# Performance work log

Hardware: AMD Instinct MI355X
Metric: run time of the kernel (lower is better)

## Reference

```python
import jax, jax.numpy as jnp
import numpy as np

N = 50000          # nodes
E = 800000         # edges (avg degree 16)
F_IN = 64          # raw node features
H = 128            # hidden width (n_hidden[0..5])
H6 = 256           # n_hidden[6]
H7 = 128           # n_hidden[7]
EDGE_DIM = 21


def _lin(k, fan_in, fan_out):
    return jax.random.normal(k, (fan_in, fan_out), jnp.float32) * (1.0 / np.sqrt(fan_in))


def setup_inputs() -> dict:
    key = jax.random.key(0)
    ks = jax.random.split(key, 32)
    inp = {
        "G": jax.random.normal(ks[0], (N, F_IN), jnp.float32),
        "edge_index": jax.random.randint(ks[1], (2, E), 0, N, jnp.int32),
        "edge_attr": jax.random.normal(ks[2], (E, EDGE_DIM), jnp.float32),
        # MLP embedding
        "We1": _lin(ks[3], F_IN, H), "be1": jnp.zeros((H,), jnp.float32),
        "We2": _lin(ks[4], H, H),    "be2": jnp.zeros((H,), jnp.float32),
        "We3": _lin(ks[5], H, H),    "be3": jnp.zeros((H,), jnp.float32),
        # conv1 (ResGatedGraphConv, edge_dim=21)
        "c1_Wk": _lin(ks[6], H, H),  "c1_bk": jnp.zeros((H,), jnp.float32),
        "c1_Wq": _lin(ks[7], H, H),  "c1_bq": jnp.zeros((H,), jnp.float32),
        "c1_Wv": _lin(ks[8], H, H),  "c1_bv": jnp.zeros((H,), jnp.float32),
        "c1_We": _lin(ks[9], EDGE_DIM, H),
        "c1_Ws": _lin(ks[10], H, H), "c1_bs": jnp.zeros((H,), jnp.float32),
        # conv2
        "c2_Wk": _lin(ks[11], H, H), "c2_bk": jnp.zeros((H,), jnp.float32),
        "c2_Wq": _lin(ks[12], H, H), "c2_bq": jnp.zeros((H,), jnp.float32),
        "c2_Wv": _lin(ks[13], H, H), "c2_bv": jnp.zeros((H,), jnp.float32),
        "c2_We": _lin(ks[14], EDGE_DIM, H),
        "c2_Ws": _lin(ks[15], H, H), "c2_bs": jnp.zeros((H,), jnp.float32),
        # graph-level MLP
        "Wg1": _lin(ks[16], H, H),   "bg1": jnp.zeros((H,), jnp.float32),
        "Wg2": _lin(ks[17], H, H),   "bg2": jnp.zeros((H,), jnp.float32),
        # head (input is concat(node_emb, graph_mean) -> 2*H)
        "Wl1": _lin(ks[18], 2 * H, H6), "bl1": jnp.zeros((H6,), jnp.float32),
        "Wl2": _lin(ks[19], H6, H7),    "bl2": jnp.zeros((H7,), jnp.float32),
        "Wl3": _lin(ks[20], H7, 1),     "bl3": jnp.zeros((1,), jnp.float32),
    }
    return inp


def _res_gated_conv(x, src, dst, ea, Wk, bk, Wq, bq, Wv, bv, We, Ws, bs):
    """PyG ResGatedGraphConv with edge_dim:
    msg = sigmoid((k_i + e) + (q_j + e)) * (v_j + e), scatter-add to target i."""
    k = x @ Wk + bk            # [N,H] keys (target side)
    q = x @ Wq + bq            # [N,H] queries (source side)
    v = x @ Wv + bv            # [N,H] values (source side)
    e = ea @ We                # [E,H] edge transform (no bias)
    gate = jax.nn.sigmoid(k[dst] + q[src] + 2.0 * e)   # [E,H]
    msg = gate * (v[src] + e)                           # [E,H]
    agg = jax.ops.segment_sum(msg, dst, num_segments=x.shape[0])
    return agg + x @ Ws + bs   # root/skip connection


def reference(G, edge_index, edge_attr,
              We1, be1, We2, be2, We3, be3,
              c1_Wk, c1_bk, c1_Wq, c1_bq, c1_Wv, c1_bv, c1_We, c1_Ws, c1_bs,
              c2_Wk, c2_bk, c2_Wq, c2_bq, c2_Wv, c2_bv, c2_We, c2_Ws, c2_bs,
              Wg1, bg1, Wg2, bg2,
              Wl1, bl1, Wl2, bl2, Wl3, bl3):
    src, dst = edge_index[0], edge_index[1]
    h = jax.nn.relu(G @ We1 + be1)
    h = jax.nn.relu(h @ We2 + be2)
    h = jax.nn.relu(h @ We3 + be3)
    h = jax.nn.relu(_res_gated_conv(h, src, dst, edge_attr,
                                    c1_Wk, c1_bk, c1_Wq, c1_bq, c1_Wv, c1_bv,
                                    c1_We, c1_Ws, c1_bs))
    h = jax.nn.relu(_res_gated_conv(h, src, dst, edge_attr,
                                    c2_Wk, c2_bk, c2_Wq, c2_bq, c2_Wv, c2_bv,
                                    c2_We, c2_Ws, c2_bs))
    h = jax.nn.relu(h @ Wg1 + bg1)
    h = h @ Wg2 + bg2                      # [N,H]
    gmean = jnp.mean(h, axis=0)            # graph embedding [H]
    u = jnp.concatenate([h, jnp.broadcast_to(gmean, h.shape)], axis=-1)  # [N,2H]
    u = jax.nn.relu(u @ Wl1 + bl1)
    u = jax.nn.relu(u @ Wl2 + bl2)
    u = (u @ Wl3 + bl3).squeeze(-1)        # [N] per-node scalar logits
    return u
```

## Files before the change

### kernel.cpp

```cpp
#include <hip/hip_runtime.h>
#include <hip/hip_fp16.h>

#define NN 50000
#define NE 800000
#define HH 128
#define SCAN_BS 512
#define SCAN_NB 98
#define LDK 40
#define LDA 136
#define LDU 264

typedef _Float16 half8 __attribute__((ext_vector_type(8)));
typedef float f32x4  __attribute__((ext_vector_type(4)));

__global__ __launch_bounds__(256)
void presplit_w(const float* __restrict__ s0,  const float* __restrict__ s1,
                const float* __restrict__ s2,  const float* __restrict__ s3,
                const float* __restrict__ s4,  const float* __restrict__ s5,
                const float* __restrict__ s6,  const float* __restrict__ s7,
                const float* __restrict__ s8,  const float* __restrict__ s9,
                const float* __restrict__ s10, const float* __restrict__ s11,
                const float* __restrict__ s12, const float* __restrict__ s13,
                const float* __restrict__ s14, _Float16* __restrict__ wps)
{
    const float* srcs[15] = {s0,s1,s2,s3,s4,s5,s6,s7,s8,s9,s10,s11,s12,s13,s14};
    const int Ks[15]   = {64,128,128,128,128,128,128,128,128,128,128,128,128,128,256};
    const int logKs[15]= { 6,  7,  7,  7,  7,  7,  7,  7,  7,  7,  7,  7,  7,  7,  8};
    const int off[15]  = {0,8192,24576,40960,57344,73728,90112,106496,122880,
                          139264,155648,172032,188416,204800,237568};

    const int mi = blockIdx.y;
    const float* src = srcs[mi];
    const int K = Ks[mi], logK = logKs[mi];
    const int N = (mi == 13) ? 256 : 128;
    _Float16* dst = wps + off[mi];
    const int tot = K * N;
    const int base = (blockIdx.x * 256 + threadIdx.x) * 4;
    if (base >= tot) return;
    const int n = base >> logK;
    const int k = base & (K - 1);
#pragma unroll
    for (int x = 0; x < 4; ++x)
        dst[(size_t)n * K + k + x] = (_Float16)src[(size_t)(k + x) * N + n];
}

template<bool RELU>
__device__ __forceinline__ void layer_l2l(
    const _Float16* __restrict__ actA, int lda, int K,
    const _Float16* __restrict__ Bt,
    const float* __restrict__ bias,
    _Float16* __restrict__ actO, int ldo, int oc0,
    _Float16* __restrict__ Bs)
{
    const int t = threadIdx.x, lane = t & 63;
    const int wr = (t >> 6) >> 1, wc = (t >> 6) & 1;
    const int fr = lane & 15, fg = lane >> 4;
    const int rb = t >> 1, kb = (t & 1) * 16;

    f32x4 acc[2][4] = {};
    for (int k0 = 0; k0 < K; k0 += 32) {
        const _Float16* p = Bt + (size_t)rb * K + k0 + kb;
        const half8 v0 = *reinterpret_cast<const half8*>(p);
        const half8 v1 = *reinterpret_cast<const half8*>(p + 8);
        *reinterpret_cast<half8*>(&Bs[rb * LDK + kb])     = v0;
        *reinterpret_cast<half8*>(&Bs[rb * LDK + kb + 8]) = v1;
        __syncthreads();

        half8 a[2], b[4];
#pragma unroll
        for (int i = 0; i < 2; ++i)
            a[i] = *reinterpret_cast<const half8*>(&actA[(wr * 32 + i * 16 + fr) * lda + k0 + fg * 8]);
#pragma unroll
        for (int j = 0; j < 4; ++j)
            b[j] = *reinterpret_cast<const half8*>(&Bs[(wc * 64 + j * 16 + fr) * LDK + fg * 8]);
#pragma unroll
        for (int i = 0; i < 2; ++i)
#pragma unroll
            for (int j = 0; j < 4; ++j)
                acc[i][j] = __builtin_amdgcn_mfma_f32_16x16x32_f16(a[i], b[j], acc[i][j], 0, 0, 0);
        __syncthreads();
    }
#pragma unroll
    for (int j = 0; j < 4; ++j) {
        const int gnl = wc * 64 + j * 16 + fr;
        const float bv = bias[gnl];
#pragma unroll
        for (int i = 0; i < 2; ++i)
#pragma unroll
            for (int rr = 0; rr < 4; ++rr) {
                float v = acc[i][j][rr] + bv;
                if (RELU) v = fmaxf(v, 0.f);
                actO[(wr * 32 + i * 16 + fg * 4 + rr) * ldo + oc0 + gnl] = (_Float16)v;
            }
    }
    __syncthreads();
}

__global__ __launch_bounds__(256)
void mlp3_kernel(const float* __restrict__ G,
                 const _Float16* __restrict__ W1, const float* __restrict__ b1,
                 const _Float16* __restrict__ W2, const float* __restrict__ b2,
                 const _Float16* __restrict__ W3, const float* __restrict__ b3,
                 _Float16* __restrict__ outf, int M)
{
    __shared__ __attribute__((aligned(16))) _Float16 AA[64 * LDA];
    __shared__ __attribute__((aligned(16))) _Float16 AB[64 * LDA];
    __shared__ __attribute__((aligned(16))) _Float16 Bs[128 * LDK];

    const int t  = threadIdx.x;
    const int m0 = blockIdx.x << 6;

    {
        const int r  = t >> 2;
        const int c0 = (t & 3) * 16;
        const int gm = m0 + r;
#pragma unroll
        for (int h = 0; h < 2; ++h) {
            float4 v0 = make_float4(0.f, 0.f, 0.f, 0.f), v1 = v0;
            if (gm < M) {
                v0 = *reinterpret_cast<const float4*>(G + (size_t)gm * 64 + c0 + h * 8);
                v1 = *reinterpret_cast<const float4*>(G + (size_t)gm * 64 + c0 + h * 8 + 4);
            }
            half8 hv;
            hv[0] = (_Float16)v0.x; hv[1] = (_Float16)v0.y;
            hv[2] = (_Float16)v0.z; hv[3] = (_Float16)v0.w;
            hv[4] = (_Float16)v1.x; hv[5] = (_Float16)v1.y;
            hv[6] = (_Float16)v1.z; hv[7] = (_Float16)v1.w;
            *reinterpret_cast<half8*>(&AA[r * LDA + c0 + h * 8]) = hv;
        }
    }
    __syncthreads();

    layer_l2l<true>(AA, LDA, 64,  W1, b1, AB, LDA, 0, Bs);
    layer_l2l<true>(AB, LDA, 128, W2, b2, AA, LDA, 0, Bs);
    layer_l2l<true>(AA, LDA, 128, W3, b3, AB, LDA, 0, Bs);

    {
        const int r  = t >> 2;
        const int c0 = (t & 3) * 32;
        const int gm = m0 + r;
        if (gm < M) {
#pragma unroll
            for (int x = 0; x < 32; x += 8)
                *reinterpret_cast<half8*>(outf + (size_t)gm * 128 + c0 + x) =
                    *reinterpret_cast<const half8*>(&AB[r * LDA + c0 + x]);
        }
    }
}

__global__ __launch_bounds__(256)
void kqvs_kernel(const _Float16* __restrict__ act,
                 const _Float16* __restrict__ B0, const _Float16* __restrict__ B1,
                 const _Float16* __restrict__ B2, const _Float16* __restrict__ B3,
                 const float* __restrict__ b0, const float* __restrict__ b1,
                 const float* __restrict__ b2, const float* __restrict__ b3,
                 _Float16* __restrict__ ksb, _Float16* __restrict__ qvb, int M)
{
    __shared__ __attribute__((aligned(16))) _Float16 AA[64 * LDA];
    __shared__ __attribute__((aligned(16))) _Float16 Bs[128 * LDK];

    const int t  = threadIdx.x, lane = t & 63;
    const int m0 = blockIdx.x << 6;
    const int wr = (t >> 6) >> 1, wc = (t >> 6) & 1;
    const int fr = lane & 15, fg = lane >> 4;
    const int rb = t >> 1, kb = (t & 1) * 16;

    {
        const int r  = t >> 2;
        const int c0 = (t & 3) * 32;
        const int gm = m0 + r;
#pragma unroll
        for (int x = 0; x < 32; x += 8) {
            half8 v = {0,0,0,0,0,0,0,0};
            if (gm < M) v = *reinterpret_cast<const half8*>(act + (size_t)gm * 128 + c0 + x);
            *reinterpret_cast<half8*>(&AA[r * LDA + c0 + x]) = v;
        }
    }
    __syncthreads();

#pragma unroll
    for (int nb = 0; nb < 4; ++nb) {
        const _Float16* Bt = (nb == 0) ? B0 : (nb == 1) ? B1 : (nb == 2) ? B2 : B3;
        const float*    bt = (nb == 0) ? b0 : (nb == 1) ? b1 : (nb == 2) ? b2 : b3;
        _Float16* dst = (nb < 2) ? ksb : qvb;
        const int sub = (nb & 1) * 2;

        f32x4 acc[2][4] = {};
        for (int k0 = 0; k0 < 128; k0 += 32) {
            const _Float16* p = Bt + (size_t)rb * 128 + k0 + kb;
            const half8 v0 = *reinterpret_cast<const half8*>(p);
            const half8 v1 = *reinterpret_cast<const half8*>(p + 8);
            *reinterpret_cast<half8*>(&Bs[rb * LDK + kb])     = v0;
            *reinterpret_cast<half8*>(&Bs[rb * LDK + kb + 8]) = v1;
            __syncthreads();

            half8 a[2], b[4];
#pragma unroll
            for (int i = 0; i < 2; ++i)
                a[i] = *reinterpret_cast<const half8*>(&AA[(wr * 32 + i * 16 + fr) * LDA + k0 + fg * 8]);
#pragma unroll
            for (int j = 0; j < 4; ++j)
                b[j] = *reinterpret_cast<const half8*>(&Bs[(wc * 64 + j * 16 + fr) * LDK + fg * 8]);
#pragma unroll
            for (int i = 0; i < 2; ++i)
#pragma unroll
                for (int j = 0; j < 4; ++j)
                    acc[i][j] = __builtin_amdgcn_mfma_f32_16x16x32_f16(a[i], b[j], acc[i][j], 0, 0, 0);
            __syncthreads();
        }
#pragma unroll
        for (int j = 0; j < 4; ++j) {
            const int gnl = wc * 64 + j * 16 + fr;
            const int pos = ((gnl >> 1) << 2) + sub + (gnl & 1);
            const float bv = bt[gnl];
#pragma unroll
            for (int i = 0; i < 2; ++i) {
                const int mbase = m0 + wr * 32 + i * 16 + fg * 4;
#pragma unroll
                for (int rr = 0; rr < 4; ++rr) {
                    const int gm = mbase + rr;
                    if (gm < M)
                        dst[(size_t)gm * 256 + pos] = (_Float16)(acc[i][j][rr] + bv);
                }
            }
        }
    }
}

__global__ __launch_bounds__(256)
void graph2_kernel(const _Float16* __restrict__ act,
                   const _Float16* __restrict__ Wg1t, const float* __restrict__ bg1,
                   const _Float16* __restrict__ Wg2t, const float* __restrict__ bg2,
                   _Float16* __restrict__ g2f, float* __restrict__ gsum, int M)
{
    __shared__ __attribute__((aligned(16))) _Float16 AA[64 * LDA];
    __shared__ __attribute__((aligned(16))) _Float16 AB[64 * LDA];
    __shared__ __attribute__((aligned(16))) _Float16 Bs[128 * LDK];

    const int t  = threadIdx.x, lane = t & 63;
    const int m0 = blockIdx.x << 6;
    const int wr = (t >> 6) >> 1, wc = (t >> 6) & 1;
    const int fr = lane & 15, fg = lane >> 4;
    const int rb = t >> 1, kb = (t & 1) * 16;

    {
        const int r  = t >> 2;
        const int c0 = (t & 3) * 32;
        const int gm = m0 + r;
#pragma unroll
        for (int x = 0; x < 32; x += 8) {
            half8 v = {0,0,0,0,0,0,0,0};
            if (gm < M) v = *reinterpret_cast<const half8*>(act + (size_t)gm * 128 + c0 + x);
            *reinterpret_cast<half8*>(&AA[r * LDA + c0 + x]) = v;
        }
    }
    __syncthreads();

    layer_l2l<true>(AA, LDA, 128, Wg1t, bg1, AB, LDA, 0, Bs);

    f32x4 acc[2][4] = {};
    for (int k0 = 0; k0 < 128; k0 += 32) {
        const _Float16* p = Wg2t + (size_t)rb * 128 + k0 + kb;
        const half8 v0 = *reinterpret_cast<const half8*>(p);
        const half8 v1 = *reinterpret_cast<const half8*>(p + 8);
        *reinterpret_cast<half8*>(&Bs[rb * LDK + kb])     = v0;
        *reinterpret_cast<half8*>(&Bs[rb * LDK + kb + 8]) = v1;
        __syncthreads();
        half8 a[2], b[4];
#pragma unroll
        for (int i = 0; i < 2; ++i)
            a[i] = *reinterpret_cast<const half8*>(&AB[(wr * 32 + i * 16 + fr) * LDA + k0 + fg * 8]);
#pragma unroll
        for (int j = 0; j < 4; ++j)
            b[j] = *reinterpret_cast<const half8*>(&Bs[(wc * 64 + j * 16 + fr) * LDK + fg * 8]);
#pragma unroll
        for (int i = 0; i < 2; ++i)
#pragma unroll
            for (int j = 0; j < 4; ++j)
                acc[i][j] = __builtin_amdgcn_mfma_f32_16x16x32_f16(a[i], b[j], acc[i][j], 0, 0, 0);
        __syncthreads();
    }
#pragma unroll
    for (int j = 0; j < 4; ++j) {
        const int gn = wc * 64 + j * 16 + fr;
        const float bv = bg2[gn];
        float csum = 0.f;
#pragma unroll
        for (int i = 0; i < 2; ++i) {
            const int mbase = m0 + wr * 32 + i * 16 + fg * 4;
#pragma unroll
            for (int rr = 0; rr < 4; ++rr) {
                const int gm = mbase + rr;
                if (gm < M) {
                    const float v = acc[i][j][rr] + bv;
                    csum += v;
                    g2f[(size_t)gm * 128 + gn] = (_Float16)v;
                }
            }
        }
        csum += __shfl_xor(csum, 16);
        csum += __shfl_xor(csum, 32);
        if (fg == 0) atomicAdd(&gsum[gn], csum);
    }
}

__global__ __launch_bounds__(256)
void head3_kernel(const _Float16* __restrict__ g2f,
                  const _Float16* __restrict__ Wl1t,
                  const float* __restrict__ gvec,
                  const _Float16* __restrict__ Wl2t,
                  const float* __restrict__ bl2,
                  const float* __restrict__ wl3,
                  const float* __restrict__ bl3,
                  float* __restrict__ out, int M)
{
    __shared__ __attribute__((aligned(16))) _Float16 AA[64 * LDA];
    __shared__ __attribute__((aligned(16))) _Float16 UB[64 * LDU];
    __shared__ __attribute__((aligned(16))) _Float16 Bs[128 * LDK];
    __shared__ float psum[2][64];

    const int t  = threadIdx.x, lane = t & 63;
    const int m0 = blockIdx.x << 6;
    const int wr = (t >> 6) >> 1, wc = (t >> 6) & 1;
    const int fr = lane & 15, fg = lane >> 4;
    const int rb = t >> 1, kb = (t & 1) * 16;

    {
        const int r  = t >> 2;
        const int c0 = (t & 3) * 32;
        const int gm = m0 + r;
#pragma unroll
        for (int x = 0; x < 32; x += 8) {
            half8 v = {0,0,0,0,0,0,0,0};
            if (gm < M) v = *reinterpret_cast<const half8*>(g2f + (size_t)gm * 128 + c0 + x);
            *reinterpret_cast<half8*>(&AA[r * LDA + c0 + x]) = v;
        }
    }
    __syncthreads();

    layer_l2l<true>(AA, LDA, 128, Wl1t,             gvec,       UB, LDU, 0,   Bs);
    layer_l2l<true>(AA, LDA, 128, Wl1t + 128 * 128, gvec + 128, UB, LDU, 128, Bs);

    f32x4 acc[2][4] = {};
    for (int k0 = 0; k0 < 256; k0 += 32) {
        const _Float16* p = Wl2t + (size_t)rb * 256 + k0 + kb;
        const half8 v0 = *reinterpret_cast<const half8*>(p);
        const half8 v1 = *reinterpret_cast<const half8*>(p + 8);
        *reinterpret_cast<half8*>(&Bs[rb * LDK + kb])     = v0;
        *reinterpret_cast<half8*>(&Bs[rb * LDK + kb + 8]) = v1;
        __syncthreads();
        half8 a[2], b[4];
#pragma unroll
        for (int i = 0; i < 2; ++i)
            a[i] = *reinterpret_cast<const half8*>(&UB[(wr * 32 + i * 16 + fr) * LDU + k0 + fg * 8]);
#pragma unroll
        for (int j = 0; j < 4; ++j)
            b[j] = *reinterpret_cast<const half8*>(&Bs[(wc * 64 + j * 16 + fr) * LDK + fg * 8]);
#pragma unroll
        for (int i = 0; i < 2; ++i)
#pragma unroll
            for (int j = 0; j < 4; ++j)
                acc[i][j] = __builtin_amdgcn_mfma_f32_16x16x32_f16(a[i], b[j], acc[i][j], 0, 0, 0);
        __syncthreads();
    }

    float p[2][4] = {};
#pragma unroll
    for (int j = 0; j < 4; ++j) {
        const int gnl = wc * 64 + j * 16 + fr;
        const float bv = bl2[gnl];
        const float wv = wl3[gnl];
#pragma unroll
        for (int i = 0; i < 2; ++i)
#pragma unroll
            for (int rr = 0; rr < 4; ++rr)
                p[i][rr] += fmaxf(acc[i][j][rr] + bv, 0.f) * wv;
    }
#pragma unroll
    for (int i = 0; i < 2; ++i)
#pragma unroll
        for (int rr = 0; rr < 4; ++rr) {
            float s = p[i][rr];
            s += __shfl_xor(s, 1);
            s += __shfl_xor(s, 2);
            s += __shfl_xor(s, 4);
            s += __shfl_xor(s, 8);
            p[i][rr] = s;
        }
    if (fr == 0) {
#pragma unroll
        for (int i = 0; i < 2; ++i)
#pragma unroll
            for (int rr = 0; rr < 4; ++rr)
                psum[wc][wr * 32 + i * 16 + fg * 4 + rr] = p[i][rr];
    }
    __syncthreads();
    if (t < 64) {
        const int gm = m0 + t;
        if (gm < M) out[gm] = psum[0][t] + psum[1][t] + bl3[0];
    }
}

__global__ __launch_bounds__(256)
void hist_kernel(const int* __restrict__ ei, int* __restrict__ deg)
{
    const int e = blockIdx.x * 256 + threadIdx.x;
    if (e < NE) atomicAdd(&deg[ei[NE + e]], 1);
}

__global__ __launch_bounds__(SCAN_BS)
void scan1_kernel(const int* __restrict__ deg, int* __restrict__ incl,
                  int* __restrict__ bsum)
{
    __shared__ int sm[SCAN_BS];
    const int t = threadIdx.x;
    const int i = blockIdx.x * SCAN_BS + t;
    sm[t] = (i < NN) ? deg[i] : 0;
    __syncthreads();
    for (int d = 1; d < SCAN_BS; d <<= 1) {
        const int add = (t >= d) ? sm[t - d] : 0;
        __syncthreads();
        sm[t] += add;
        __syncthreads();
    }
    if (i < NN) incl[i] = sm[t];
    if (t == SCAN_BS - 1) bsum[blockIdx.x] = sm[t];
}

__global__ __launch_bounds__(128)
void scan2_kernel(int* __restrict__ bsum)
{
    __shared__ int sm[128];
    const int t = threadIdx.x;
    const int v = (t < SCAN_NB) ? bsum[t] : 0;
    sm[t] = v;
    __syncthreads();
    for (int d = 1; d < 128; d <<= 1) {
        const int add = (t >= d) ? sm[t - d] : 0;
        __syncthreads();
        sm[t] += add;
        __syncthreads();
    }
    if (t < SCAN_NB) bsum[t] = sm[t] - v;
}

__global__ __launch_bounds__(SCAN_BS)
void scan3_kernel(const int* __restrict__ incl, const int* __restrict__ deg,
                  const int* __restrict__ bsum, int* __restrict__ offs)
{
    const int t = threadIdx.x;
    const int i = blockIdx.x * SCAN_BS + t;
    if (i < NN) offs[i] = incl[i] - deg[i] + bsum[blockIdx.x];
    if (i == 0) offs[NN] = NE;
}

__global__ __launch_bounds__(256)
void scatter_kernel(const int* __restrict__ ei, const int* __restrict__ offs,
                    int* __restrict__ cur,
                    int* __restrict__ csr_src, int* __restrict__ csr_eid)
{
    const int e = blockIdx.x * 256 + threadIdx.x;
    if (e >= NE) return;
    const int d = ei[NE + e];
    const int p = offs[d] + atomicAdd(&cur[d], 1);
    csr_src[p] = ei[e];
    csr_eid[p] = e;
}

__global__ __launch_bounds__(256)
void build_ea2(const int* __restrict__ csr_eid, const float* __restrict__ ea,
               unsigned* __restrict__ ea2)
{
    const int j = blockIdx.x * 256 + threadIdx.x;
    if (j >= NE) return;
    const int eid = csr_eid[j];
    const float* src = ea + (size_t)eid * 21;
    unsigned* dst = ea2 + (size_t)j * 21;
#pragma unroll
    for (int q = 0; q < 21; ++q) {
        const __half2 h = __floats2half2_rn(src[q], src[q]);
        dst[q] = __builtin_bit_cast(unsigned, h);
    }
}

__global__ __launch_bounds__(256, 8)
void conv_agg_kernel(const int* __restrict__ offs,
                     const int* __restrict__ csr_src,
                     const unsigned* __restrict__ ea2,
                     const float* __restrict__ We,
                     const _Float16* __restrict__ ksb,
                     const _Float16* __restrict__ qvb,
                     _Float16* __restrict__ outh)
{
    const int t    = threadIdx.x;
    const int lane = t & 63;
    const int n    = blockIdx.x * 4 + (t >> 6);
    if (n >= NN) return;

    __half2 w2[21];
#pragma unroll
    for (int q = 0; q < 21; ++q) {
        const float2 wq = *reinterpret_cast<const float2*>(&We[q * HH + 2 * lane]);
        w2[q] = __floats2half2_rn(wq.x, wq.y);
    }

    const uint2 ks = *reinterpret_cast<const uint2*>(ksb + (size_t)n * 256 + lane * 4);
    const __half2 k2 = __builtin_bit_cast(__half2, ks.x);
    const __half2 s2 = __builtin_bit_cast(__half2, ks.y);
    const __half2 one2 = __float2half2_rn(1.f);
    const __half2 two2 = __float2half2_rn(2.f);

    const int j0 = __builtin_amdgcn_readfirstlane(offs[n]);
    const int j1 = __builtin_amdgcn_readfirstlane(offs[n + 1]);
    float acc0 = 0.f, acc1 = 0.f;

#define GATHER(S) (*reinterpret_cast<const uint2*>(qvb + (size_t)(S) * 256 + lane * 4))

#define EDGE(QV, J) { \
    const __half2* aa_ = reinterpret_cast<const __half2*>(ea2 + (size_t)(J) * 21); \
    __half2 e01_ = __float2half2_rn(0.f); \
    _Pragma("unroll") \
    for (int q_ = 0; q_ < 21; ++q_) e01_ = __hfma2(aa_[q_], w2[q_], e01_); \
    const __half2 q2_ = __builtin_bit_cast(__half2, (QV).x); \
    const __half2 v2_ = __builtin_bit_cast(__half2, (QV).y); \
    const __half2 g_  = __hadd2(k2, __hfma2(two2, e01_, q2_)); \
    const __half2 ex_ = h2exp(__hneg2(g_)); \
    const __half2 gate_ = h2rcp(__hadd2(one2, ex_)); \
    const __half2 m_ = __hmul2(gate_, __hadd2(v2_, e01_)); \
    acc0 += __low2float(m_); \
    acc1 += __high2float(m_); }

    int j = j0;
    for (; j + 4 <= j1; j += 4) {
        const int sa = csr_src[j],     sb = csr_src[j + 1];
        const int sc = csr_src[j + 2], sd = csr_src[j + 3];
        const uint2 qva = GATHER(sa);
        const uint2 qvb_ = GATHER(sb);
        const uint2 qvc = GATHER(sc);
        const uint2 qvd = GATHER(sd);
        EDGE(qva, j)
        EDGE(qvb_, j + 1)
        EDGE(qvc, j + 2)
        EDGE(qvd, j + 3)
    }
    for (; j < j1; ++j) {
        const int s_ = csr_src[j];
        const uint2 qv = GATHER(s_);
        EDGE(qv, j)
    }
#undef GATHER
#undef EDGE

    const float r0 = fmaxf(acc0 + __low2float(s2), 0.f);
    const float r1 = fmaxf(acc1 + __high2float(s2), 0.f);
    const __half2 res = __floats2half2_rn(r0, r1);
    *reinterpret_cast<__half2*>(outh + (size_t)n * HH + 2 * lane) = res;
}

__global__ __launch_bounds__(256)
void gvec_kernel(const float* __restrict__ gsum,
                 const float* __restrict__ Wl1,
                 const float* __restrict__ bl1,
                 float* __restrict__ gvec, float invM)
{
    const int j = threadIdx.x;
    float acc = bl1[j];
    for (int k = 0; k < 128; ++k)
        acc += (gsum[k] * invM) * Wl1[(size_t)(128 + k) * 256 + j];
    gvec[j] = acc;
}

extern "C" void kernel_launch(void* const* d_in, const int* in_sizes, int n_in,
                              void* d_out, int out_size, void* d_ws, size_t ws_size,
                              hipStream_t stream)
{
    const float* G   = (const float*)d_in[0];
    const int*   ei  = (const int*)  d_in[1];
    const float* ea  = (const float*)d_in[2];
    const float* We1 = (const float*)d_in[3];  const float* be1 = (const float*)d_in[4];
    const float* We2 = (const float*)d_in[5];  const float* be2 = (const float*)d_in[6];
    const float* We3 = (const float*)d_in[7];  const float* be3 = (const float*)d_in[8];
    const float* c1_Wk = (const float*)d_in[9];  const float* c1_bk = (const float*)d_in[10];
    const float* c1_Wq = (const float*)d_in[11]; const float* c1_bq = (const float*)d_in[12];
    const float* c1_Wv = (const float*)d_in[13]; const float* c1_bv = (const float*)d_in[14];
    const float* c1_We = (const float*)d_in[15];
    const float* c1_Ws = (const float*)d_in[16]; const float* c1_bs = (const float*)d_in[17];
    const float* c2_Wk = (const float*)d_in[18]; const float* c2_bk = (const float*)d_in[19];
    const float* c2_Wq = (const float*)d_in[20]; const float* c2_bq = (const float*)d_in[21];
    const float* c2_Wv = (const float*)d_in[22]; const float* c2_bv = (const float*)d_in[23];
    const float* c2_We = (const float*)d_in[24];
    const float* c2_Ws = (const float*)d_in[25]; const float* c2_bs = (const float*)d_in[26];
    const float* Wg1 = (const float*)d_in[27]; const float* bg1 = (const float*)d_in[28];
    const float* Wg2 = (const float*)d_in[29]; const float* bg2 = (const float*)d_in[30];
    const float* Wl1 = (const float*)d_in[31]; const float* bl1 = (const float*)d_in[32];
    const float* Wl2 = (const float*)d_in[33]; const float* bl2 = (const float*)d_in[34];
    const float* Wl3 = (const float*)d_in[35]; const float* bl3 = (const float*)d_in[36];

    float* out = (float*)d_out;

    char* ws = (char*)d_ws;
    size_t off = 0;
    _Float16* wps  = (_Float16*)(ws + off); off += 270336 * 2;
    _Float16* hA   = (_Float16*)(ws + off); off += (size_t)NN * 128 * 2;
    _Float16* hB   = (_Float16*)(ws + off); off += (size_t)NN * 128 * 2;
    _Float16* ksb  = (_Float16*)(ws + off); off += (size_t)NN * 256 * 2;
    _Float16* qvb  = (_Float16*)(ws + off); off += (size_t)NN * 256 * 2;
    unsigned* ea2  = (unsigned*)(ws + off); off += (size_t)NE * 21 * 4;
    int*      deg  = (int*)     (ws + off); off += (size_t)NN * 4;
    int*      cur  = (int*)     (ws + off); off += (size_t)NN * 4;
    float*    gsum = (float*)   (ws + off); off += 256 * 4;
    float*    gvec = (float*)   (ws + off); off += 256 * 4;
    int*      incl = (int*)     (ws + off); off += (size_t)NN * 4;
    int*      bsum = (int*)     (ws + off); off += 128 * 4;
    int*      offs = (int*)     (ws + off); off += (size_t)(NN + 2) * 4;
    int*      csr_src = (int*)  (ws + off); off += (size_t)NE * 4;
    int*      csr_eid = (int*)  (ws + off); off += (size_t)NE * 4;

    const int O_We1 = 0,      O_We2 = 8192,   O_We3 = 24576;
    const int O_c1k = 40960,  O_c1s = 57344,  O_c1q = 73728,  O_c1v = 90112;
    const int O_c2k = 106496, O_c2s = 122880, O_c2q = 139264, O_c2v = 155648;
    const int O_Wg1 = 172032, O_Wg2 = 188416, O_Wl1 = 204800, O_Wl2 = 237568;

    const dim3 blk(256);
    const int  MT = (NN + 63) / 64;
    const int  EB = (NE + 255) / 256;
    const int  AGGB = (NN + 3) / 4;

    presplit_w<<<dim3(32, 15), blk, 0, stream>>>(
        We1, We2, We3, c1_Wk, c1_Ws, c1_Wq, c1_Wv,
        c2_Wk, c2_Ws, c2_Wq, c2_Wv, Wg1, Wg2, Wl1, Wl2, wps);

    hipMemsetAsync(deg, 0, (size_t)(2 * NN + 256) * 4, stream);
    hist_kernel<<<dim3(EB), blk, 0, stream>>>(ei, deg);
    scan1_kernel<<<dim3(SCAN_NB), dim3(SCAN_BS), 0, stream>>>(deg, incl, bsum);
    scan2_kernel<<<dim3(1), dim3(128), 0, stream>>>(bsum);
    scan3_kernel<<<dim3(SCAN_NB), dim3(SCAN_BS), 0, stream>>>(incl, deg, bsum, offs);
    scatter_kernel<<<dim3(EB), blk, 0, stream>>>(ei, offs, cur, csr_src, csr_eid);
    build_ea2<<<dim3(EB), blk, 0, stream>>>(csr_eid, ea, ea2);

    mlp3_kernel<<<dim3(MT), blk, 0, stream>>>(G,
        wps + O_We1, be1, wps + O_We2, be2, wps + O_We3, be3, hA, NN);

    kqvs_kernel<<<dim3(MT), blk, 0, stream>>>(hA,
        wps + O_c1k, wps + O_c1s, wps + O_c1q, wps + O_c1v,
        c1_bk, c1_bs, c1_bq, c1_bv, ksb, qvb, NN);
    conv_agg_kernel<<<dim3(AGGB), blk, 0, stream>>>(offs, csr_src, ea2, c1_We,
        ksb, qvb, hB);

    kqvs_kernel<<<dim3(MT), blk, 0, stream>>>(hB,
        wps + O_c2k, wps + O_c2s, wps + O_c2q, wps + O_c2v,
        c2_bk, c2_bs, c2_bq, c2_bv, ksb, qvb, NN);
    conv_agg_kernel<<<dim3(AGGB), blk, 0, stream>>>(offs, csr_src, ea2, c2_We,
        ksb, qvb, hA);

    graph2_kernel<<<dim3(MT), blk, 0, stream>>>(hA,
        wps + O_Wg1, bg1, wps + O_Wg2, bg2, hB, gsum, NN);

    gvec_kernel<<<dim3(1), dim3(256), 0, stream>>>(gsum, Wl1, bl1, gvec, 1.f / NN);

    head3_kernel<<<dim3(MT), blk, 0, stream>>>(hB,
        wps + O_Wl1, gvec, wps + O_Wl2, bl2, Wl3, bl3, out, NN);
}
```

Measured before the change: 516.1 us.

## Merge graph-prep kernels with weight split and MLP, fold sigmoid into exp2

Merges the degree histogram into the weight-presplit launch, and merges the CSR scatter and edge-attribute conversion into the MLP embedding launch as extra blocks. Each edge now writes its converted attributes straight to its CSR slot, which removes the csr_eid array, one kernel and two launches. The k and q projections are pre-scaled by -log2(e), so the gate uses exp2 with no negation. This drops an instruction per edge, but the ea2 writes become scattered and the scaled values run through fp16 with a little more rounding.

```diff
diff --git a/kernel.cpp b/kernel.cpp
--- a/kernel.cpp
+++ b/kernel.cpp
@@ -9,33 +9,42 @@
 #define LDK 40
 #define LDA 136
 #define LDU 264
+#define EBLK ((NE + 255) / 256)
 
 typedef _Float16 half8 __attribute__((ext_vector_type(8)));
 typedef float f32x4  __attribute__((ext_vector_type(4)));
 
 __global__ __launch_bounds__(256)
-void presplit_w(const float* __restrict__ s0,  const float* __restrict__ s1,
-                const float* __restrict__ s2,  const float* __restrict__ s3,
-                const float* __restrict__ s4,  const float* __restrict__ s5,
-                const float* __restrict__ s6,  const float* __restrict__ s7,
-                const float* __restrict__ s8,  const float* __restrict__ s9,
-                const float* __restrict__ s10, const float* __restrict__ s11,
-                const float* __restrict__ s12, const float* __restrict__ s13,
-                const float* __restrict__ s14, _Float16* __restrict__ wps)
-{
+void prep_kernel(const float* __restrict__ s0,  const float* __restrict__ s1,
+                 const float* __restrict__ s2,  const float* __restrict__ s3,
+                 const float* __restrict__ s4,  const float* __restrict__ s5,
+                 const float* __restrict__ s6,  const float* __restrict__ s7,
+                 const float* __restrict__ s8,  const float* __restrict__ s9,
+                 const float* __restrict__ s10, const float* __restrict__ s11,
+                 const float* __restrict__ s12, const float* __restrict__ s13,
+                 const float* __restrict__ s14, _Float16* __restrict__ wps,
+                 const int* __restrict__ ei, int* __restrict__ deg)
+{
+    const int b = blockIdx.x;
+    if (b >= 480) {
+        const int e = (b - 480) * 256 + threadIdx.x;
+        if (e < NE) atomicAdd(&deg[ei[NE + e]], 1);
+        return;
+    }
     const float* srcs[15] = {s0,s1,s2,s3,s4,s5,s6,s7,s8,s9,s10,s11,s12,s13,s14};
     const int Ks[15]   = {64,128,128,128,128,128,128,128,128,128,128,128,128,128,256};
     const int logKs[15]= { 6,  7,  7,  7,  7,  7,  7,  7,  7,  7,  7,  7,  7,  7,  8};
     const int off[15]  = {0,8192,24576,40960,57344,73728,90112,106496,122880,
                           139264,155648,172032,188416,204800,237568};
 
-    const int mi = blockIdx.y;
+    const int mi = b >> 5;
+    const int bx = b & 31;
     const float* src = srcs[mi];
     const int K = Ks[mi], logK = logKs[mi];
     const int N = (mi == 13) ? 256 : 128;
     _Float16* dst = wps + off[mi];
     const int tot = K * N;
-    const int base = (blockIdx.x * 256 + threadIdx.x) * 4;
+    const int base = (bx * 256 + threadIdx.x) * 4;
     if (base >= tot) return;
     const int n = base >> logK;
     const int k = base & (K - 1);
@@ -66,18 +75,18 @@
         *reinterpret_cast<half8*>(&Bs[rb * LDK + kb + 8]) = v1;
         __syncthreads();
 
-        half8 a[2], b[4];
+        half8 a[2], bfr[4];
 #pragma unroll
         for (int i = 0; i < 2; ++i)
             a[i] = *reinterpret_cast<const half8*>(&actA[(wr * 32 + i * 16 + fr) * lda + k0 + fg * 8]);
 #pragma unroll
         for (int j = 0; j < 4; ++j)
-            b[j] = *reinterpret_cast<const half8*>(&Bs[(wc * 64 + j * 16 + fr) * LDK + fg * 8]);
+            bfr[j] = *reinterpret_cast<const half8*>(&Bs[(wc * 64 + j * 16 + fr) * LDK + fg * 8]);
 #pragma unroll
         for (int i = 0; i < 2; ++i)
 #pragma unroll
             for (int j = 0; j < 4; ++j)
-                acc[i][j] = __builtin_amdgcn_mfma_f32_16x16x32_f16(a[i], b[j], acc[i][j], 0, 0, 0);
+                acc[i][j] = __builtin_amdgcn_mfma_f32_16x16x32_f16(a[i], bfr[j], acc[i][j], 0, 0, 0);
         __syncthreads();
     }
 #pragma unroll
@@ -97,19 +106,37 @@
 }
 
 __global__ __launch_bounds__(256)
-void mlp3_kernel(const float* __restrict__ G,
-                 const _Float16* __restrict__ W1, const float* __restrict__ b1,
-                 const _Float16* __restrict__ W2, const float* __restrict__ b2,
-                 const _Float16* __restrict__ W3, const float* __restrict__ b3,
-                 _Float16* __restrict__ outf, int M)
+void phase5_kernel(const int* __restrict__ ei, const int* __restrict__ offs,
+                   int* __restrict__ cur, const float* __restrict__ ea,
+                   int* __restrict__ csr_src, unsigned* __restrict__ ea2,
+                   const float* __restrict__ G,
+                   const _Float16* __restrict__ W1, const float* __restrict__ b1,
+                   const _Float16* __restrict__ W2, const float* __restrict__ b2,
+                   const _Float16* __restrict__ W3, const float* __restrict__ b3,
+                   _Float16* __restrict__ outf, int M)
 {
     __shared__ __attribute__((aligned(16))) _Float16 AA[64 * LDA];
     __shared__ __attribute__((aligned(16))) _Float16 AB[64 * LDA];
     __shared__ __attribute__((aligned(16))) _Float16 Bs[128 * LDK];
 
-    const int t  = threadIdx.x;
-    const int m0 = blockIdx.x << 6;
-
+    const int t = threadIdx.x;
+    if (blockIdx.x < EBLK) {
+        const int e = blockIdx.x * 256 + t;
+        if (e >= NE) return;
+        const int d = ei[NE + e];
+        const int p = offs[d] + atomicAdd(&cur[d], 1);
+        csr_src[p] = ei[e];
+        const float* src = ea + (size_t)e * 21;
+        unsigned* dst = ea2 + (size_t)p * 21;
+#pragma unroll
+        for (int q = 0; q < 21; ++q) {
+            const __half2 h = __floats2half2_rn(src[q], src[q]);
+            dst[q] = __builtin_bit_cast(unsigned, h);
+        }
+        return;
+    }
+
+    const int m0 = (blockIdx.x - EBLK) << 6;
     {
         const int r  = t >> 2;
         const int c0 = (t & 3) * 16;
@@ -184,6 +211,7 @@
         const float*    bt = (nb == 0) ? b0 : (nb == 1) ? b1 : (nb == 2) ? b2 : b3;
         _Float16* dst = (nb < 2) ? ksb : qvb;
         const int sub = (nb & 1) * 2;
+        const float scl = (nb == 0 || nb == 2) ? -1.44269504f : 1.0f;
 
         f32x4 acc[2][4] = {};
         for (int k0 = 0; k0 < 128; k0 += 32) {
@@ -220,7 +248,7 @@
                 for (int rr = 0; rr < 4; ++rr) {
                     const int gm = mbase + rr;
                     if (gm < M)
-                        dst[(size_t)gm * 256 + pos] = (_Float16)(acc[i][j][rr] + bv);
+                        dst[(size_t)gm * 256 + pos] = (_Float16)((acc[i][j][rr] + bv) * scl);
                 }
             }
         }
@@ -401,13 +429,6 @@
     }
 }
 
-__global__ __launch_bounds__(256)
-void hist_kernel(const int* __restrict__ ei, int* __restrict__ deg)
-{
-    const int e = blockIdx.x * 256 + threadIdx.x;
-    if (e < NE) atomicAdd(&deg[ei[NE + e]], 1);
-}
-
 __global__ __launch_bounds__(SCAN_BS)
 void scan1_kernel(const int* __restrict__ deg, int* __restrict__ incl,
                   int* __restrict__ bsum)
@@ -452,35 +473,6 @@
     const int i = blockIdx.x * SCAN_BS + t;
     if (i < NN) offs[i] = incl[i] - deg[i] + bsum[blockIdx.x];
     if (i == 0) offs[NN] = NE;
-}
-
-__global__ __launch_bounds__(256)
-void scatter_kernel(const int* __restrict__ ei, const int* __restrict__ offs,
-                    int* __restrict__ cur,
-                    int* __restrict__ csr_src, int* __restrict__ csr_eid)
-{
-    const int e = blockIdx.x * 256 + threadIdx.x;
-    if (e >= NE) return;
-    const int d = ei[NE + e];
-    const int p = offs[d] + atomicAdd(&cur[d], 1);
-    csr_src[p] = ei[e];
-    csr_eid[p] = e;
-}
-
-__global__ __launch_bounds__(256)
-void build_ea2(const int* __restrict__ csr_eid, const float* __restrict__ ea,
-               unsigned* __restrict__ ea2)
-{
-    const int j = blockIdx.x * 256 + threadIdx.x;
-    if (j >= NE) return;
-    const int eid = csr_eid[j];
-    const float* src = ea + (size_t)eid * 21;
-    unsigned* dst = ea2 + (size_t)j * 21;
-#pragma unroll
-    for (int q = 0; q < 21; ++q) {
-        const __half2 h = __floats2half2_rn(src[q], src[q]);
-        dst[q] = __builtin_bit_cast(unsigned, h);
-    }
 }
 
 __global__ __launch_bounds__(256, 8)
@@ -508,7 +500,7 @@
     const __half2 k2 = __builtin_bit_cast(__half2, ks.x);
     const __half2 s2 = __builtin_bit_cast(__half2, ks.y);
     const __half2 one2 = __float2half2_rn(1.f);
-    const __half2 two2 = __float2half2_rn(2.f);
+    const __half2 cm2  = __float2half2_rn(-2.88539008f);
 
     const int j0 = __builtin_amdgcn_readfirstlane(offs[n]);
     const int j1 = __builtin_amdgcn_readfirstlane(offs[n + 1]);
@@ -523,9 +515,8 @@
     for (int q_ = 0; q_ < 21; ++q_) e01_ = __hfma2(aa_[q_], w2[q_], e01_); \
     const __half2 q2_ = __builtin_bit_cast(__half2, (QV).x); \
     const __half2 v2_ = __builtin_bit_cast(__half2, (QV).y); \
-    const __half2 g_  = __hadd2(k2, __hfma2(two2, e01_, q2_)); \
-    const __half2 ex_ = h2exp(__hneg2(g_)); \
-    const __half2 gate_ = h2rcp(__hadd2(one2, ex_)); \
+    const __half2 arg_ = __hadd2(k2, __hfma2(cm2, e01_, q2_)); \
+    const __half2 gate_ = h2rcp(__hadd2(one2, h2exp2(arg_))); \
     const __half2 m_ = __hmul2(gate_, __hadd2(v2_, e01_)); \
     acc0 += __low2float(m_); \
     acc1 += __high2float(m_); }
@@ -614,7 +605,6 @@
     int*      bsum = (int*)     (ws + off); off += 128 * 4;
     int*      offs = (int*)     (ws + off); off += (size_t)(NN + 2) * 4;
     int*      csr_src = (int*)  (ws + off); off += (size_t)NE * 4;
-    int*      csr_eid = (int*)  (ws + off); off += (size_t)NE * 4;
 
     const int O_We1 = 0,      O_We2 = 8192,   O_We3 = 24576;
     const int O_c1k = 40960,  O_c1s = 57344,  O_c1q = 73728,  O_c1v = 90112;
@@ -623,22 +613,19 @@
 
     const dim3 blk(256);
     const int  MT = (NN + 63) / 64;
-    const int  EB = (NE + 255) / 256;
     const int  AGGB = (NN + 3) / 4;
 
-    presplit_w<<<dim3(32, 15), blk, 0, stream>>>(
+    hipMemsetAsync(deg, 0, (size_t)(2 * NN + 256) * 4, stream);
+    prep_kernel<<<dim3(480 + EBLK), blk, 0, stream>>>(
         We1, We2, We3, c1_Wk, c1_Ws, c1_Wq, c1_Wv,
-        c2_Wk, c2_Ws, c2_Wq, c2_Wv, Wg1, Wg2, Wl1, Wl2, wps);
-
-    hipMemsetAsync(deg, 0, (size_t)(2 * NN + 256) * 4, stream);
-    hist_kernel<<<dim3(EB), blk, 0, stream>>>(ei, deg);
+        c2_Wk, c2_Ws, c2_Wq, c2_Wv, Wg1, Wg2, Wl1, Wl2, wps, ei, deg);
+
     scan1_kernel<<<dim3(SCAN_NB), dim3(SCAN_BS), 0, stream>>>(deg, incl, bsum);
     scan2_kernel<<<dim3(1), dim3(128), 0, stream>>>(bsum);
     scan3_kernel<<<dim3(SCAN_NB), dim3(SCAN_BS), 0, stream>>>(incl, deg, bsum, offs);
-    scatter_kernel<<<dim3(EB), blk, 0, stream>>>(ei, offs, cur, csr_src, csr_eid);
-    build_ea2<<<dim3(EB), blk, 0, stream>>>(csr_eid, ea, ea2);
-
-    mlp3_kernel<<<dim3(MT), blk, 0, stream>>>(G,
+
+    phase5_kernel<<<dim3(EBLK + MT), blk, 0, stream>>>(
+        ei, offs, cur, ea, csr_src, ea2, G,
         wps + O_We1, be1, wps + O_We2, be2, wps + O_We3, be3, hA, NN);
 
     kqvs_kernel<<<dim3(MT), blk, 0, stream>>>(hA,
```

Result: faster. 454.9 us (-11.9%).
